# Kernel tuning notes

Measured on AMD Instinct MI355X. Metric: run time of the kernel, lower is better.

## Reference

```python
import jax, jax.numpy as jnp
import numpy as np

B, S, D, H = 8, 1024, 1024, 16  # batch, seq (queries==keys), d_model, heads
DH = D // H


def setup_inputs() -> dict:
    key = jax.random.key(0)
    ks = jax.random.split(key, 7)
    return {
        "query": jax.random.normal(ks[0], (B, S, D), dtype=jnp.float32),
        "key": jax.random.normal(ks[1], (B, S, D), dtype=jnp.float32),
        "value": jax.random.normal(ks[2], (B, S, D), dtype=jnp.float32),
        "valid_len": jax.random.randint(ks[3], (B, S), 0, S, dtype=jnp.int32),
        "Wq": jax.random.normal(ks[4], (D, D), dtype=jnp.float32) / np.sqrt(D),
        "Wk": jax.random.normal(ks[5], (D, D), dtype=jnp.float32) / np.sqrt(D),
        "Wv": jax.random.normal(ks[6], (D, D), dtype=jnp.float32) / np.sqrt(D),
    }


def reference(query, key, value, valid_len, Wq, Wk, Wv):
    b, sq, _ = query.shape
    sk = key.shape[1]
    # projections (bias-free Linear), then split hidden into H contiguous chunks per head
    q = (query @ Wq).reshape(b, sq, H, DH)  # [B,Sq,H,dh]
    k = (key @ Wk).reshape(b, sk, H, DH)
    v = (value @ Wv).reshape(b, sk, H, DH)
    scale = 1.0 / jnp.sqrt(jnp.asarray(DH, dtype=q.dtype))
    scores = jnp.einsum("bqhd,bkhd->bhqk", q, k) * scale  # [B,H,Sq,Sk]
    # per-query mask (valid_len.dim()==2 path): key index < valid_len[b, q]
    col = jnp.arange(sk)
    mask = col[None, None, None, :] < valid_len[:, None, :, None]  # [B,1,Sq,Sk]
    scores = jnp.where(mask, scores, jnp.asarray(-1000.0, dtype=scores.dtype))
    prob = jax.nn.softmax(scores, axis=-1)
    out = jnp.einsum("bhqk,bkhd->bqhd", prob, v)  # [B,Sq,H,dh]
    return out.reshape(b, sq, D)
```

## Files before the change

### kernel.cpp

```cpp
#include <hip/hip_runtime.h>
#include <hip/hip_bf16.h>
#include <stdint.h>


#define B_  8
#define S_  1024
#define D_  1024
#define H_  16
#define DH_ 64

typedef short bf16x8 __attribute__((ext_vector_type(8)));
typedef float f32x4  __attribute__((ext_vector_type(4)));
typedef unsigned short u16;
typedef uint32_t u32;
typedef u16 u16x8 __attribute__((ext_vector_type(8)));
typedef u16 u16x4 __attribute__((ext_vector_type(4)));

#define MASKVAL  (-1442.6950408889634f)
#define QSCALE   (0.18033688011112042f)

union U4 { u32 u[4]; bf16x8 v; };

__device__ __forceinline__ u16 f2bf(float f) {
    union { float f; uint32_t u; } v; v.f = f;
    uint32_t u = v.u;
    return (u16)((u + 0x7FFFu + ((u >> 16) & 1u)) >> 16);
}

__device__ __forceinline__ u32 cvtpk(float lo, float hi) {
    u32 r;
    asm("v_cvt_pk_bf16_f32 %0, %1, %2" : "=v"(r) : "v"(lo), "v"(hi));
    return r;
}

__device__ __forceinline__ void gload16(const void* g, const void* l) {
    __builtin_amdgcn_global_load_lds(
        (const __attribute__((address_space(1))) void*)g,
        (__attribute__((address_space(3))) void*)l, 16, 0, 0);
}

__device__ __forceinline__ float xor32max(float v) {
    float a = v, b = v;
    asm volatile("" : "+v"(b));
    asm("v_permlane32_swap_b32 %0, %1" : "+v"(a), "+v"(b));
    return fmaxf(a, b);
}
__device__ __forceinline__ float xor32add(float v) {
    float a = v, b = v;
    asm volatile("" : "+v"(b));
    asm("v_permlane32_swap_b32 %0, %1" : "+v"(a), "+v"(b));
    return a + b;
}

__global__ void transpose_w3_kernel(const float* __restrict__ Wq, const float* __restrict__ Wk,
                                    const float* __restrict__ Wv, u16* __restrict__ Wts) {
    __shared__ u16 tile[32 * 33];
    const int z = blockIdx.z;
    const float* W = (z == 0) ? Wq : (z == 1) ? Wk : Wv;
    u16* Wt = Wts + (size_t)z * D_ * D_;
    int k0 = blockIdx.y * 32, n0 = blockIdx.x * 32;
    int t = threadIdx.x;
    int c = t & 31;
    for (int p = 0; p < 4; ++p) {
        int r = p * 8 + (t >> 5);
        tile[r * 33 + c] = f2bf(W[(size_t)(k0 + r) * D_ + n0 + c]);
    }
    __syncthreads();
    int rn = t >> 3, c4 = t & 7;
    u16x4 v;
    for (int j = 0; j < 4; ++j) v[j] = tile[(c4 * 4 + j) * 33 + rn];
    *(u16x4*)(Wt + (size_t)(n0 + rn) * D_ + k0 + c4 * 4) = v;
}

__global__ __launch_bounds__(1024) void sort_vlen_kernel(const int* __restrict__ vlen,
                                                         int* __restrict__ qidx) {
    __shared__ u32 sk[1024];
    const int b = blockIdx.x, t = threadIdx.x;
    int k = vlen[b * S_ + t];
    u32 key = (k == 0) ? (u32)S_ : (u32)k;
    sk[t] = (key << 10) | (u32)t;
    __syncthreads();
    for (int sz = 2; sz <= 1024; sz <<= 1) {
        for (int st = sz >> 1; st > 0; st >>= 1) {
            int j = t ^ st;
            if (j > t) {
                u32 a = sk[t], c = sk[j];
                bool des = (t & sz) != 0;
                if ((a > c) != des) { sk[t] = c; sk[j] = a; }
            }
            __syncthreads();
        }
    }
    qidx[b * S_ + t] = (int)(sk[t] & 1023u);
}

__global__ __launch_bounds__(256) void gemm_qkv_kernel(const float* __restrict__ Aq,
                                                       const float* __restrict__ Ak,
                                                       const float* __restrict__ Av,
                                                       const u16* __restrict__ wts,
                                                       u16* __restrict__ qb, u16* __restrict__ kb,
                                                       u16* __restrict__ vb) {
    __shared__ float lds_a[2][128 * 32];
    __shared__ u16  lds_b[2][128 * 32];
    const int zy = blockIdx.y;
    const int z = zy >> 3;
    const float* A = (z == 0) ? Aq : (z == 1) ? Ak : Av;
    const u16* Bt = wts + (size_t)z * D_ * D_;
    u16* C = (z == 0) ? qb : (z == 1) ? kb : vb;
    const float cmul = (z == 0) ? QSCALE : 1.0f;

    const int t = threadIdx.x, w = t >> 6, l = t & 63;
    const int m0 = blockIdx.x * 128, n0 = (zy & 7) * 128;
    const int wr = w >> 1, wc = w & 1;
    const int l15 = l & 15, l4 = l >> 4;
    f32x4 acc[4][4] = {};

    auto stage = [&](int buf, int kt) {
        int k0 = kt * 32;
        #pragma unroll
        for (int i = 0; i < 4; ++i) {
            int c = i * 256 + t;
            int row = c >> 3, xs = (c & 7) ^ (row & 7);
            gload16(A + (size_t)(m0 + row) * D_ + k0 + xs * 4, &lds_a[buf][c * 4]);
        }
        #pragma unroll
        for (int i = 0; i < 2; ++i) {
            int c = i * 256 + t;
            int row = c >> 2, xc = (c & 3) ^ (row & 3);
            gload16(Bt + (size_t)(n0 + row) * D_ + k0 + xc * 8, &lds_b[buf][c * 8]);
        }
    };

    stage(0, 0);
    __syncthreads();
    int buf = 0;
    for (int kt = 0; kt < 32; ++kt) {
        if (kt + 1 < 32) stage(buf ^ 1, kt + 1);
        bf16x8 af[4], bfr[4];
        #pragma unroll
        for (int mi = 0; mi < 4; ++mi) {
            int r = wr * 64 + mi * 16 + l15;
            int c0 = (l4 * 2) ^ (r & 7), c1 = (l4 * 2 + 1) ^ (r & 7);
            float4 fa0 = *(const float4*)&lds_a[buf][r * 32 + c0 * 4];
            float4 fa1 = *(const float4*)&lds_a[buf][r * 32 + c1 * 4];
            U4 d;
            d.u[0] = cvtpk(fa0.x, fa0.y); d.u[1] = cvtpk(fa0.z, fa0.w);
            d.u[2] = cvtpk(fa1.x, fa1.y); d.u[3] = cvtpk(fa1.z, fa1.w);
            af[mi] = d.v;
        }
        #pragma unroll
        for (int ni = 0; ni < 4; ++ni) {
            int r = wc * 64 + ni * 16 + l15;
            bfr[ni] = *(const bf16x8*)&lds_b[buf][r * 32 + ((l4 ^ (r & 3)) * 8)];
        }
        #pragma unroll
        for (int mi = 0; mi < 4; ++mi)
            #pragma unroll
            for (int ni = 0; ni < 4; ++ni)
                acc[mi][ni] = __builtin_amdgcn_mfma_f32_16x16x32_bf16(af[mi], bfr[ni], acc[mi][ni], 0, 0, 0);
        __syncthreads();
        buf ^= 1;
    }
    #pragma unroll
    for (int mi = 0; mi < 4; ++mi)
        #pragma unroll
        for (int ni = 0; ni < 4; ++ni)
            #pragma unroll
            for (int r = 0; r < 4; ++r) {
                int m = m0 + wr * 64 + mi * 16 + l4 * 4 + r;
                int n = n0 + wc * 64 + ni * 16 + l15;
                C[(size_t)m * D_ + n] = f2bf(acc[mi][ni][r] * cmul);
            }
}

__global__ void transpose_v_kernel(const u16* __restrict__ vb, u16* __restrict__ vt) {
    __shared__ u16 t2[64 * 72];
    int bid = blockIdx.x;
    int st = bid & 15, bh = bid >> 4;
    int b = bh >> 4, h = bh & 15;
    int t = threadIdx.x;
    for (int p = 0; p < 2; ++p) {
        int c = p * 256 + t, r = c >> 3, x = c & 7;
        u16x8 val = *(const u16x8*)&vb[((size_t)(b * S_ + st * 64 + r)) * D_ + h * 64 + x * 8];
        *(u16x8*)&t2[r * 72 + x * 8] = val;
    }
    __syncthreads();
    int d = t >> 2, kc = t & 3;
    u16x8 o0, o1;
    for (int j = 0; j < 8; ++j) o0[j] = t2[(kc * 16 + j) * 72 + d];
    for (int j = 0; j < 8; ++j) o1[j] = t2[(kc * 16 + 8 + j) * 72 + d];
    size_t obase = ((size_t)bh * 64 + d) * (size_t)S_ + st * 64 + kc * 16;
    *(u16x8*)&vt[obase] = o0;
    *(u16x8*)&vt[obase + 8] = o1;
}

__global__ __launch_bounds__(512) void attn_kernel(const u16* __restrict__ qb,
                                                   const u16* __restrict__ kb,
                                                   const u16* __restrict__ vt,
                                                   const int* __restrict__ vlen,
                                                   const int* __restrict__ qidx,
                                                   float* __restrict__ out) {
    __shared__ __align__(16) char smem_raw[34816];
    auto kv = [&](int buf, int which) -> u16* {
        return (u16*)(smem_raw + buf * 16384 + which * 8192);
    };

    const int t = threadIdx.x, w = t >> 6, l = t & 63;
    const int n = blockIdx.x;
    const int x = n & 7, j = n >> 3;
    const int bh = x + 8 * (j >> 2);
    const int p = j & 3;
    const int b = bh >> 4, h = bh & 15;
    const int l15 = l & 15, l4 = l >> 4;
    const bool rowe = ((l & 16) == 0);

    const u16* kbase = kb + ((size_t)(b * S_)) * D_ + h * 64;
    const u16* vbase = vt + ((size_t)bh * 64) * (size_t)S_;

    const int kr_s = t >> 3, x_s = (t & 7) ^ (kr_s & 7);
    auto stage = [&](int buf, int kt) {
        gload16(kbase + (size_t)(kt * 64 + kr_s) * D_ + x_s * 8, &kv(buf, 0)[t * 8]);
        gload16(vbase + (size_t)kr_s * S_ + kt * 64 + x_s * 8, &kv(buf, 1)[t * 8]);
    };

    auto redist = [&](u32 P, u32 Q, u32& oe, u32& oo) {
        u32 X = P, Y = Q;
        asm("v_permlane32_swap_b32 %0, %1" : "+v"(X), "+v"(Y));
        u32 t1 = (u32)__shfl_xor((int)Y, 16, 64);
        u32 t2 = (u32)__shfl_xor((int)X, 16, 64);
        oe = rowe ? X : t1;
        oo = rowe ? t2 : Y;
    };

    auto wavemax = [&](int v) {
        int s1 = __shfl_xor(v, 1, 64);  v = v > s1 ? v : s1;
        int s2 = __shfl_xor(v, 2, 64);  v = v > s2 ? v : s2;
        int s4 = __shfl_xor(v, 4, 64);  v = v > s4 ? v : s4;
        int s8 = __shfl_xor(v, 8, 64);  v = v > s8 ? v : s8;
        return v;
    };

    const int q0a = (7 - p) * 128, q0b = p * 128;

    const int qia = qidx[b * S_ + q0a + w * 16 + l15];
    const u16* qpa = qb + ((size_t)(b * S_ + qia)) * D_ + h * 64 + l4 * 8;
    const bf16x8 bqa0 = *(const bf16x8*)qpa;
    const bf16x8 bqa1 = *(const bf16x8*)(qpa + 32);
    const int vla = vlen[b * S_ + qia];

    const int qib = qidx[b * S_ + q0b + w * 16 + l15];
    const u16* qpb = qb + ((size_t)(b * S_ + qib)) * D_ + h * 64 + l4 * 8;
    const bf16x8 bqb0 = *(const bf16x8*)qpb;
    const bf16x8 bqb1 = *(const bf16x8*)(qpb + 32);
    const int vlb = vlen[b * S_ + qib];

    int mk = vlen[b * S_ + qidx[b * S_ + q0a + 127]];
    if (mk == 0) mk = S_;
    const int nkt = (mk + 63) >> 6;

    const int nktwa = (wavemax(vla == 0 ? S_ : vla) + 63) >> 6;
    const int nktwb = (wavemax(vlb == 0 ? S_ : vlb) + 63) >> 6;

    float ma = -3.0e38f, lsa = 0.f, mb = -3.0e38f, lsb = 0.f;
    f32x4 acca[4] = {}, accb[4] = {};

    auto process = [&](int buf, int kt, const bf16x8& bq0, const bf16x8& bq1, int vlq,
                       float& m, float& lsum, f32x4 (&acc)[4]) {
        f32x4 sc[4];
        __builtin_amdgcn_s_setprio(1);
        #pragma unroll
        for (int nf = 0; nf < 4; ++nf) {
            int kr = nf * 16 + l15, swz = kr & 7;
            bf16x8 ak0 = *(const bf16x8*)&kv(buf, 0)[kr * 64 + ((l4 ^ swz) * 8)];
            bf16x8 ak1 = *(const bf16x8*)&kv(buf, 0)[kr * 64 + (((l4 + 4) ^ swz) * 8)];
            f32x4 s = {0.f, 0.f, 0.f, 0.f};
            s = __builtin_amdgcn_mfma_f32_16x16x32_bf16(ak0, bq0, s, 0, 0, 0);
            s = __builtin_amdgcn_mfma_f32_16x16x32_bf16(ak1, bq1, s, 0, 0, 0);
            sc[nf] = s;
        }
        __builtin_amdgcn_s_setprio(0);

        const int thr = vlq - kt * 64 - 4 * l4;
        float pv[16];
        float pm = -3.0e38f;
        if (__all(thr >= 52)) {
            #pragma unroll
            for (int nf = 0; nf < 4; ++nf)
                #pragma unroll
                for (int r = 0; r < 4; ++r) {
                    float y = sc[nf][r];
                    pv[nf * 4 + r] = y;
                    pm = fmaxf(pm, y);
                }
        } else {
            #pragma unroll
            for (int nf = 0; nf < 4; ++nf)
                #pragma unroll
                for (int r = 0; r < 4; ++r) {
                    float y = ((nf * 16 + r) < thr) ? sc[nf][r] : MASKVAL;
                    pv[nf * 4 + r] = y;
                    pm = fmaxf(pm, y);
                }
        }
        pm = fmaxf(pm, __shfl_xor(pm, 16, 64));
        pm = xor32max(pm);
        if (!__all(pm - m <= 8.0f)) {
            float mn = fmaxf(m, pm);
            float corr = __builtin_amdgcn_exp2f(m - mn);
            m = mn;
            lsum *= corr;
            #pragma unroll
            for (int df = 0; df < 4; ++df) acc[df] *= corr;
        }
        float rs = 0.f;
        #pragma unroll
        for (int i = 0; i < 16; ++i) {
            float e = __builtin_amdgcn_exp2f(pv[i] - m);
            pv[i] = e;
            rs += e;
        }
        rs += __shfl_xor(rs, 16, 64);
        rs = xor32add(rs);
        lsum += rs;

        u32 pw[8];
        #pragma unroll
        for (int nf = 0; nf < 4; ++nf) {
            pw[2 * nf]     = cvtpk(pv[4 * nf + 0], pv[4 * nf + 1]);
            pw[2 * nf + 1] = cvtpk(pv[4 * nf + 2], pv[4 * nf + 3]);
        }
        U4 pb0, pb1;
        redist(pw[0], pw[2], pb0.u[0], pb0.u[2]);
        redist(pw[1], pw[3], pb0.u[1], pb0.u[3]);
        redist(pw[4], pw[6], pb1.u[0], pb1.u[2]);
        redist(pw[5], pw[7], pb1.u[1], pb1.u[3]);

        __builtin_amdgcn_s_setprio(1);
        #pragma unroll
        for (int df = 0; df < 4; ++df) {
            int vr = df * 16 + l15, swz = vr & 7;
            bf16x8 av0 = *(const bf16x8*)&kv(buf, 1)[vr * 64 + ((l4 ^ swz) * 8)];
            bf16x8 av1 = *(const bf16x8*)&kv(buf, 1)[vr * 64 + (((l4 + 4) ^ swz) * 8)];
            acc[df] = __builtin_amdgcn_mfma_f32_16x16x32_bf16(av0, pb0.v, acc[df], 0, 0, 0);
            acc[df] = __builtin_amdgcn_mfma_f32_16x16x32_bf16(av1, pb1.v, acc[df], 0, 0, 0);
        }
        __builtin_amdgcn_s_setprio(0);
    };

    stage(0, 0);
    __syncthreads();

    int buf = 0;
    for (int kt = 0; kt < nkt; ++kt) {
        if (kt + 1 < nkt) stage(buf ^ 1, kt + 1);
        if (kt < nktwa) process(buf, kt, bqa0, bqa1, vla, ma, lsa, acca);
        if (kt < nktwb) process(buf, kt, bqb0, bqb1, vlb, mb, lsb, accb);
        __syncthreads();
        buf ^= 1;
    }

    float* ep = (float*)smem_raw;
    {
        const float inv = 1.0f / lsa;
        #pragma unroll
        for (int df = 0; df < 4; ++df)
            #pragma unroll
            for (int r = 0; r < 4; ++r)
                ep[w * 1088 + l15 * 68 + df * 16 + 4 * l4 + r] = acca[df][r] * inv;
        __syncthreads();
        #pragma unroll
        for (int rr = 0; rr < 4; ++rr) {
            int row = l4 * 4 + rr;
            int qi2 = qidx[b * S_ + q0a + w * 16 + row];
            float4 vv = *(float4*)&ep[w * 1088 + row * 68 + l15 * 4];
            *(float4*)&out[((size_t)(b * S_ + qi2)) * D_ + h * 64 + l15 * 4] = vv;
        }
        __syncthreads();
    }
    {
        const float inv = 1.0f / lsb;
        #pragma unroll
        for (int df = 0; df < 4; ++df)
            #pragma unroll
            for (int r = 0; r < 4; ++r)
                ep[w * 1088 + l15 * 68 + df * 16 + 4 * l4 + r] = accb[df][r] * inv;
        __syncthreads();
        #pragma unroll
        for (int rr = 0; rr < 4; ++rr) {
            int row = l4 * 4 + rr;
            int qi2 = qidx[b * S_ + q0b + w * 16 + row];
            float4 vv = *(float4*)&ep[w * 1088 + row * 68 + l15 * 4];
            *(float4*)&out[((size_t)(b * S_ + qi2)) * D_ + h * 64 + l15 * 4] = vv;
        }
    }
}

extern "C" void kernel_launch(void* const* d_in, const int* in_sizes, int n_in,
                              void* d_out, int out_size, void* d_ws, size_t ws_size,
                              hipStream_t stream) {
    const float* query = (const float*)d_in[0];
    const float* key   = (const float*)d_in[1];
    const float* value = (const float*)d_in[2];
    const int*   vlen  = (const int*)d_in[3];
    const float* Wq    = (const float*)d_in[4];
    const float* Wk    = (const float*)d_in[5];
    const float* Wv    = (const float*)d_in[6];
    float* out = (float*)d_out;

    char* ws = (char*)d_ws;
    const size_t MB = 1024 * 1024;
    const size_t TSZ = (size_t)B_ * S_ * D_ * 2;
    u16* wts = (u16*)(ws);
    u16* vt  = (u16*)(ws + 6 * MB);
    u16* qb  = (u16*)(ws + 6 * MB + TSZ);
    u16* kb  = (u16*)(ws + 6 * MB + 2 * TSZ);
    u16* vb  = (u16*)(ws + 6 * MB + 3 * TSZ);
    int* qidx = (int*)(ws + 6 * MB + 4 * TSZ);

    dim3 blk(256);

    transpose_w3_kernel<<<dim3(32, 32, 3), blk, 0, stream>>>(Wq, Wk, Wv, wts);
    sort_vlen_kernel<<<B_, dim3(1024), 0, stream>>>(vlen, qidx);

    gemm_qkv_kernel<<<dim3(64, 24), blk, 0, stream>>>(query, key, value, wts, qb, kb, vb);

    transpose_v_kernel<<<B_ * H_ * (S_ / 64), blk, 0, stream>>>(vb, vt);

    attn_kernel<<<dim3(512), dim3(512), 0, stream>>>(qb, kb, vt, vlen, qidx, out);
}
```

Before: 163.9 us.

## Convert QKV GEMM A tile to bf16 during staging via register prefetch

The QKV projection GEMM no longer copies fp32 activations straight from global memory into LDS. It prefetches the next tile into registers, converts the A tile to bf16 once, and writes both A and B tiles into LDS with a new swizzle after the MFMAs. This halves the LDS footprint for A and stops each wave from re-converting fp32 to bf16 on every fragment read. The cost is more live registers and an LDS write on the critical path before the barrier, in place of the asynchronous direct-to-LDS loads.

```diff
diff --git a/kernel.cpp b/kernel.cpp
--- a/kernel.cpp
+++ b/kernel.cpp
@@ -100,8 +100,8 @@
                                                        const u16* __restrict__ wts,
                                                        u16* __restrict__ qb, u16* __restrict__ kb,
                                                        u16* __restrict__ vb) {
-    __shared__ float lds_a[2][128 * 32];
-    __shared__ u16  lds_b[2][128 * 32];
+    __shared__ u16 lds_a[2][128 * 32];
+    __shared__ u16 lds_b[2][128 * 32];
     const int zy = blockIdx.y;
     const int z = zy >> 3;
     const float* A = (z == 0) ? Aq : (z == 1) ? Ak : Av;
@@ -115,49 +115,56 @@
     const int l15 = l & 15, l4 = l >> 4;
     f32x4 acc[4][4] = {};
 
-    auto stage = [&](int buf, int kt) {
-        int k0 = kt * 32;
-        #pragma unroll
-        for (int i = 0; i < 4; ++i) {
-            int c = i * 256 + t;
-            int row = c >> 3, xs = (c & 7) ^ (row & 7);
-            gload16(A + (size_t)(m0 + row) * D_ + k0 + xs * 4, &lds_a[buf][c * 4]);
-        }
-        #pragma unroll
-        for (int i = 0; i < 2; ++i) {
-            int c = i * 256 + t;
-            int row = c >> 2, xc = (c & 3) ^ (row & 3);
-            gload16(Bt + (size_t)(n0 + row) * D_ + k0 + xc * 8, &lds_b[buf][c * 8]);
-        }
-    };
-
-    stage(0, 0);
+    const int srow = t >> 1, shalf = t & 1;
+    const int ssw = (srow >> 1) & 3;
+    const float* agp = A + (size_t)(m0 + srow) * D_ + shalf * 16;
+    const u16*  bgp = Bt + (size_t)(n0 + srow) * D_ + shalf * 16;
+    const int ac0 = (srow * 4 + ((2 * shalf)     ^ ssw)) * 8;
+    const int ac1 = (srow * 4 + ((2 * shalf + 1) ^ ssw)) * 8;
+
+    float4 fa[4];
+    float4 fb[2];
+    auto loadg = [&](int kt) {
+        const float4* ap = (const float4*)(agp + kt * 32);
+        fa[0] = ap[0]; fa[1] = ap[1]; fa[2] = ap[2]; fa[3] = ap[3];
+        const float4* bp = (const float4*)(bgp + (size_t)kt * 32);
+        fb[0] = bp[0]; fb[1] = bp[1];
+    };
+    auto writes = [&](int buf) {
+        U4 d0, d1;
+        d0.u[0] = cvtpk(fa[0].x, fa[0].y); d0.u[1] = cvtpk(fa[0].z, fa[0].w);
+        d0.u[2] = cvtpk(fa[1].x, fa[1].y); d0.u[3] = cvtpk(fa[1].z, fa[1].w);
+        d1.u[0] = cvtpk(fa[2].x, fa[2].y); d1.u[1] = cvtpk(fa[2].z, fa[2].w);
+        d1.u[2] = cvtpk(fa[3].x, fa[3].y); d1.u[3] = cvtpk(fa[3].z, fa[3].w);
+        *(bf16x8*)&lds_a[buf][ac0] = d0.v;
+        *(bf16x8*)&lds_a[buf][ac1] = d1.v;
+        *(float4*)&lds_b[buf][ac0] = fb[0];
+        *(float4*)&lds_b[buf][ac1] = fb[1];
+    };
+
+    loadg(0);
+    writes(0);
     __syncthreads();
     int buf = 0;
     for (int kt = 0; kt < 32; ++kt) {
-        if (kt + 1 < 32) stage(buf ^ 1, kt + 1);
+        if (kt + 1 < 32) loadg(kt + 1);
         bf16x8 af[4], bfr[4];
         #pragma unroll
         for (int mi = 0; mi < 4; ++mi) {
             int r = wr * 64 + mi * 16 + l15;
-            int c0 = (l4 * 2) ^ (r & 7), c1 = (l4 * 2 + 1) ^ (r & 7);
-            float4 fa0 = *(const float4*)&lds_a[buf][r * 32 + c0 * 4];
-            float4 fa1 = *(const float4*)&lds_a[buf][r * 32 + c1 * 4];
-            U4 d;
-            d.u[0] = cvtpk(fa0.x, fa0.y); d.u[1] = cvtpk(fa0.z, fa0.w);
-            d.u[2] = cvtpk(fa1.x, fa1.y); d.u[3] = cvtpk(fa1.z, fa1.w);
-            af[mi] = d.v;
+            af[mi] = *(const bf16x8*)&lds_a[buf][(r * 4 + (l4 ^ ((r >> 1) & 3))) * 8];
         }
         #pragma unroll
         for (int ni = 0; ni < 4; ++ni) {
             int r = wc * 64 + ni * 16 + l15;
-            bfr[ni] = *(const bf16x8*)&lds_b[buf][r * 32 + ((l4 ^ (r & 3)) * 8)];
+            bfr[ni] = *(const bf16x8*)&lds_b[buf][(r * 4 + (l4 ^ ((r >> 1) & 3))) * 8];
         }
         #pragma unroll
         for (int mi = 0; mi < 4; ++mi)
             #pragma unroll
             for (int ni = 0; ni < 4; ++ni)
                 acc[mi][ni] = __builtin_amdgcn_mfma_f32_16x16x32_bf16(af[mi], bfr[ni], acc[mi][ni], 0, 0, 0);
+        if (kt + 1 < 32) writes(buf ^ 1);
         __syncthreads();
         buf ^= 1;
     }
```

Result: slower. 214.2 us (+30.7%).
